# Optimization experiments

Hardware: AMD Instinct MI355X
Metric: run time of the kernel (lower is better)

Reference implementation:

```python
import jax, jax.numpy as jnp
import numpy as np

HEADS, DIM_HEAD, K_NN, EMB = 4, 64, 16, 256
INNER = HEADS * DIM_HEAD  # 256
POS_HID = 64
ATTN_HID = 4 * DIM_HEAD  # per-head hidden of grouped 1x1 conv MLP


def setup_inputs() -> dict:
    key = jax.random.key(0)
    ks = jax.random.split(key, 16)
    b, n = 2, 4096
    s = 0.05
    inp = {
        "x": jax.random.normal(ks[0], (b, n, EMB), jnp.float32),
        "mask": jnp.ones((b, n), dtype=bool),
        "pos": jax.random.normal(ks[1], (b, n, 3), jnp.float32),
        # to_qkv (no bias)
        "Wqkv": jax.random.normal(ks[2], (EMB, 3 * INNER), jnp.float32) * s,
        # pos_mlp: Linear(3,64) -> ReLU -> Linear(64, inner)
        "Wp1": jax.random.normal(ks[3], (3, POS_HID), jnp.float32) * s,
        "bp1": jax.random.normal(ks[4], (POS_HID,), jnp.float32) * s,
        "Wp2": jax.random.normal(ks[5], (POS_HID, INNER), jnp.float32) * s,
        "bp2": jax.random.normal(ks[6], (INNER,), jnp.float32) * s,
        # attn_mlp: grouped 1x1 convs == per-head linears [h, d_in, d_out]
        "Wa1": jax.random.normal(ks[7], (HEADS, DIM_HEAD, ATTN_HID), jnp.float32) * s,
        "ba1": jax.random.normal(ks[8], (HEADS, ATTN_HID), jnp.float32) * s,
        "Wa2": jax.random.normal(ks[9], (HEADS, ATTN_HID, DIM_HEAD), jnp.float32) * s,
        "ba2": jax.random.normal(ks[10], (HEADS, DIM_HEAD), jnp.float32) * s,
        # to_out
        "Wo": jax.random.normal(ks[11], (INNER, EMB), jnp.float32) * s,
        "bo": jax.random.normal(ks[12], (EMB,), jnp.float32) * s,
    }
    return inp


def reference(x, mask, pos, Wqkv, Wp1, bp1, Wp2, bp2, Wa1, ba1, Wa2, ba2, Wo, bo):
    b, n, _ = x.shape
    h, dh = HEADS, DIM_HEAD

    qkv = x @ Wqkv                              # [b, n, 3*inner]
    q, k, v = jnp.split(qkv, 3, axis=-1)
    to_heads = lambda t: t.reshape(b, n, h, dh).transpose(0, 2, 1, 3)  # [b,h,n,d]
    q, k, v = to_heads(q), to_heads(k), to_heads(v)

    # kNN on pos (per batch, squared euclidean, includes self)
    sq = jnp.sum(pos * pos, axis=-1)
    d2 = sq[:, :, None] + sq[:, None, :] - 2.0 * jnp.einsum('bid,bjd->bij', pos, pos)
    idx = jax.lax.top_k(-d2, K_NN)[1]            # [b, n, K]

    gat_h = jax.vmap(lambda t, i: t[:, i])       # [h,n,d],[n,K] -> [h,n,K,d]
    gat = jax.vmap(lambda t, i: t[i])            # [n,c],[n,K]  -> [n,K,c]

    qg = gat_h(q, idx)                           # [b,h,n,K,d]
    kg = gat_h(k, idx)
    vg = gat_h(v, idx)

    rel = gat(pos, idx) - pos[:, :, None, :]     # [b,n,K,3]
    rpe = jax.nn.relu(rel @ Wp1 + bp1) @ Wp2 + bp2               # [b,n,K,inner]
    rpe = rpe.reshape(b, n, K_NN, h, dh).transpose(0, 3, 1, 2, 4)  # [b,h,n,K,d]

    attn_in = qg - kg + rpe                      # [b,h,n,K,d]
    hid = jax.nn.relu(jnp.einsum('bhnkd,hde->bhnke', attn_in, Wa1)
                      + ba1[None, :, None, None, :])
    sim = (jnp.einsum('bhnke,hed->bhnkd', hid, Wa2)
           + ba2[None, :, None, None, :])        # [b,h,n,K,d]

    mg = jax.vmap(lambda m, i: m[i])(mask, idx)  # [b,n,K]
    pair = (mask[:, :, None] & mg)[:, None, :, :, None]
    sim = jnp.where(pair, sim, -jnp.finfo(sim.dtype).max)

    attn = jax.nn.softmax(sim, axis=3)           # over neighbors j
    # F.normalize over dim=-2 of [b,(h d),i,j] == over the point axis i
    attn = attn / jnp.maximum(jnp.linalg.norm(attn, axis=2, keepdims=True), 1e-12)

    agg = jnp.sum(attn * (vg + rpe), axis=3)     # [b,h,n,d]
    agg = agg.transpose(0, 2, 1, 3).reshape(b, n, h * dh)
    return agg @ Wo + bo
```

## Files before the change

kernel.cpp:

```cpp
#include <hip/hip_runtime.h>
#include <float.h>

typedef unsigned int uint;
typedef unsigned short ushort;

typedef _Float16 f16x8 __attribute__((ext_vector_type(8)));
typedef float f32x4 __attribute__((ext_vector_type(4)));
#define MFMA_F16(A, B, C) __builtin_amdgcn_mfma_f32_16x16x32_f16(A, B, C, 0, 0, 0)

__device__ __forceinline__ ushort f2h(float f) {
    _Float16 h = (_Float16)f;
    return __builtin_bit_cast(ushort, h);
}
__device__ __forceinline__ float h2f(ushort u) {
    _Float16 h = __builtin_bit_cast(_Float16, u);
    return (float)h;
}
__device__ __forceinline__ uint pack2(float a, float b) {
    return (uint)f2h(a) | ((uint)f2h(b) << 16);
}
__device__ __forceinline__ uint pkrtz(float a, float b) {
    return __builtin_bit_cast(uint, __builtin_amdgcn_cvt_pkrtz(a, b));
}
__device__ __forceinline__ f16x8 cast8(uint4 u) {
    return __builtin_bit_cast(f16x8, u);
}

template <int CTRL>
__device__ __forceinline__ void dpp_min(float& v, int& j) {
    int vp = __builtin_amdgcn_update_dpp(__float_as_int(v), __float_as_int(v),
                                         CTRL, 0xF, 0xF, false);
    int jp = __builtin_amdgcn_update_dpp(j, j, CTRL, 0xF, 0xF, false);
    float vf = __int_as_float(vp);
    bool better = (vf < v) || (vf == v && jp < j);
    v = better ? vf : v;
    j = better ? jp : j;
}
__device__ __forceinline__ void wave_min(float& v, int& j) {
    dpp_min<0x121>(v, j);
    dpp_min<0x122>(v, j);
    dpp_min<0x124>(v, j);
    dpp_min<0x128>(v, j);
    float ov = __shfl_xor(v, 16);
    int oj = __shfl_xor(j, 16);
    bool better = (ov < v) || (ov == v && oj < j);
    v = better ? ov : v;
    j = better ? oj : j;
    ov = __shfl_xor(v, 32);
    oj = __shfl_xor(j, 32);
    better = (ov < v) || (ov == v && oj < j);
    v = better ? ov : v;
    j = better ? oj : j;
}

__global__ void prep_kernel(const float* __restrict__ Wqkv, const float* __restrict__ Wa1,
                            const float* __restrict__ Wa2, const float* __restrict__ Wo,
                            const float* __restrict__ Wp2, const float* __restrict__ ba1,
                            ushort* __restrict__ WcatT, ushort* __restrict__ Wa1T,
                            ushort* __restrict__ Wa2T, ushort* __restrict__ WoT,
                            ushort* __restrict__ Wp2T, ushort* __restrict__ ba1p) {
    int t = blockIdx.x * 256 + threadIdx.x;
    {
        int cc2 = t >> 8, kk = t & 255;
        float val;
        if (cc2 < 256) val = Wqkv[kk * 768 + cc2] - Wqkv[kk * 768 + 256 + cc2];
        else           val = Wqkv[kk * 768 + 256 + cc2];
        WcatT[t] = f2h(val);
    }
    if (t < 65536) {
        int hh = t >> 14, r = t & 16383;
        int e = r >> 6, kin = r & 63;
        Wa1T[t] = f2h(Wa1[((size_t)(hh * 64 + kin)) * 256 + e]);
        int d = r >> 8, pos = r & 255;
        int ec = pos >> 5, lg = (pos >> 3) & 3, q = pos & 7;
        int e2 = ec * 32 + ((q >> 2) & 1) * 16 + lg * 4 + (q & 3);
        Wa2T[t] = f2h(Wa2[((size_t)(hh * 256 + e2)) * 64 + d]);
        int c3 = t >> 8, k3 = t & 255;
        WoT[t] = f2h(Wo[k3 * 256 + c3]);
    }
    if (t < 16384) {
        int row = t >> 6, p = t & 63;
        int h = row >> 6, s = row & 63;
        int ct = s >> 4, rr = s & 15;
        int d = (ct >> 1) * 32 + ((rr >> 2) & 3) * 8 + (ct & 1) * 4 + (rr & 3);
        Wp2T[t] = f2h(Wp2[p * 256 + h * 64 + d]);
    }
    if (t < 1024) {
        int h = t >> 8, pos = t & 255;
        int ec = pos >> 5, lg = (pos >> 3) & 3, q = pos & 7;
        int e2 = ec * 32 + ((q >> 2) & 1) * 16 + lg * 4 + (q & 3);
        ba1p[t] = f2h(ba1[h * 256 + e2]);
    }
}

__global__ void pos4_kernel(const float* __restrict__ pos, float4* __restrict__ pos4) {
    int t = blockIdx.x * 256 + threadIdx.x;
    float x = pos[t * 3 + 0], y = pos[t * 3 + 1], z = pos[t * 3 + 2];
    float4 o = {x, y, z, x * x + y * y + z * z};
    pos4[t] = o;
}

template <int MODE>
__global__ __launch_bounds__(256)
void hgemm(const void* __restrict__ Av, const ushort* __restrict__ Bt,
           const float* __restrict__ bias, void* __restrict__ C0v, ushort* __restrict__ C1h) {
    __shared__ ushort Af[64 * 40];
    __shared__ ushort Bf[128 * 40];
    const int tid = threadIdx.x;
    const int l = tid & 63, wv = tid >> 6;
    const int lg = l >> 4, lr = l & 15;
    const int row0 = blockIdx.x * 64, col0 = blockIdx.y * 128;
    const int mrow = (wv >> 1) * 32, ncol = (wv & 1) * 64;
    f32x4 acc[2][4];
#pragma unroll
    for (int mt = 0; mt < 2; ++mt)
#pragma unroll
        for (int nt = 0; nt < 4; ++nt) acc[mt][nt] = (f32x4){0.f, 0.f, 0.f, 0.f};

    for (int kk = 0; kk < 256; kk += 32) {
        if (MODE == 0) {
            const float* A = (const float*)Av;
            int r = tid >> 2, kq = (tid & 3) * 8;
            float4 a0 = *(const float4*)&A[(size_t)(row0 + r) * 256 + kk + kq];
            float4 a1 = *(const float4*)&A[(size_t)(row0 + r) * 256 + kk + kq + 4];
            uint4 u;
            u.x = pack2(a0.x, a0.y); u.y = pack2(a0.z, a0.w);
            u.z = pack2(a1.x, a1.y); u.w = pack2(a1.z, a1.w);
            *(uint4*)&Af[r * 40 + kq] = u;
        } else {
            const ushort* Ah = (const ushort*)Av;
            int r = tid >> 2, kq = (tid & 3) * 8;
            *(uint4*)&Af[r * 40 + kq] = *(const uint4*)&Ah[(size_t)(row0 + r) * 256 + kk + kq];
        }
        {
            int r = tid >> 1, hh = (tid & 1) * 16;
            const uint4* src = (const uint4*)&Bt[(size_t)(col0 + r) * 256 + kk + hh];
            uint4 b0 = src[0], b1 = src[1];
            *(uint4*)&Bf[r * 40 + hh] = b0;
            *(uint4*)&Bf[r * 40 + hh + 8] = b1;
        }
        __syncthreads();
        f16x8 afr[2], bfr[4];
#pragma unroll
        for (int mt = 0; mt < 2; ++mt)
            afr[mt] = *(const f16x8*)&Af[(mrow + mt * 16 + lr) * 40 + lg * 8];
#pragma unroll
        for (int nt = 0; nt < 4; ++nt)
            bfr[nt] = *(const f16x8*)&Bf[(ncol + nt * 16 + lr) * 40 + lg * 8];
#pragma unroll
        for (int mt = 0; mt < 2; ++mt)
#pragma unroll
            for (int nt = 0; nt < 4; ++nt)
                acc[mt][nt] = MFMA_F16(afr[mt], bfr[nt], acc[mt][nt]);
        __syncthreads();
    }
#pragma unroll
    for (int mt = 0; mt < 2; ++mt)
#pragma unroll
        for (int nt = 0; nt < 4; ++nt)
#pragma unroll
            for (int j = 0; j < 4; ++j) {
                int m = row0 + mrow + mt * 16 + lg * 4 + j;
                int n = col0 + ncol + nt * 16 + lr;
                float v = acc[mt][nt][j];
                if (MODE == 1) {
                    ((float*)C0v)[(size_t)m * 256 + n] = v + bias[n];
                } else {
                    int b = m >> 12, i2 = m & 4095;
                    if (n < 256) {
                        int hh = n >> 6, d = n & 63;
                        ((ushort*)C0v)[((size_t)((b * 4 + hh) << 12) + i2) * 64 + d] = f2h(v);
                    } else {
                        int n2 = n - 256;
                        int hh = n2 >> 6, d = n2 & 63;
                        C1h[((size_t)((b * 4 + hh) << 12) + i2) * 64 + d] = f2h(v);
                    }
                }
            }
}

__global__ __launch_bounds__(256, 6)
void knn_kernel(const float4* __restrict__ pos4, int* __restrict__ idx_out) {
    const int tid = threadIdx.x;
    const int lane = tid & 63, wv = tid >> 6;
    const int pblk = blockIdx.x;
    const int b = pblk >> 10;
    const int i = ((pblk & 1023) << 2) + wv;
    const float4* p4 = pos4 + (size_t)b * 4096;
    float4 pi = p4[i];
    float xi = pi.x, yi = pi.y, zi = pi.z, sqi = pi.w;
    const int SENT = 0x7fffffff;

    float v1[4], v2[4];
    int j1[4], j2[4];
#pragma unroll
    for (int g = 0; g < 4; ++g) { v1[g] = FLT_MAX; v2[g] = FLT_MAX; j1[g] = SENT; j2[g] = SENT; }
#pragma unroll 4
    for (int m = 0; m < 64; ++m) {
        int j = m * 64 + lane;
        float4 pj = p4[j];
        float v = sqi + pj.w - 2.f * (xi * pj.x + yi * pj.y + zi * pj.z);
        int g = m & 3;
        bool bb1 = (v < v1[g]) || (v == v1[g] && j < j1[g]);
        bool bb2 = (v < v2[g]) || (v == v2[g] && j < j2[g]);
        float nv2 = bb1 ? v1[g] : (bb2 ? v : v2[g]);
        int   nj2 = bb1 ? j1[g] : (bb2 ? j : j2[g]);
        v1[g] = bb1 ? v : v1[g];
        j1[g] = bb1 ? j : j1[g];
        v2[g] = nv2;
        j2[g] = nj2;
    }
    auto mergef = [](float& a1, int& aj1, float& a2, int& aj2,
                     float b1v, int bj1, float b2v, int bj2) {
        bool aFirst = (a1 < b1v) || (a1 == b1v && aj1 < bj1);
        float r1 = aFirst ? a1 : b1v;
        int rj1 = aFirst ? aj1 : bj1;
        float cand = aFirst ? a2 : b2v;
        int candj = aFirst ? aj2 : bj2;
        float oth = aFirst ? b1v : a1;
        int othj = aFirst ? bj1 : aj1;
        bool second = (cand < oth) || (cand == oth && candj < othj);
        a1 = r1; aj1 = rj1;
        a2 = second ? cand : oth;
        aj2 = second ? candj : othj;
    };
    mergef(v1[0], j1[0], v2[0], j2[0], v1[1], j1[1], v2[1], j2[1]);
    mergef(v1[2], j1[2], v2[2], j2[2], v1[3], j1[3], v2[3], j2[3]);
    mergef(v1[0], j1[0], v2[0], j2[0], v1[2], j1[2], v2[2], j2[2]);
    float c1v = v1[0], c2v = v2[0];
    int c1j = j1[0], c2j = j2[0];

    unsigned long long extr = 0ull;
    int keep = 0;
#pragma unroll 1
    for (int r = 0; r < 16; ++r) {
        float bv = c1v;
        int bj = c1j;
        wave_min(bv, bj);
        if (lane == r) keep = bj;
        int c = bj & 63;
        if (lane == (bj >> 6)) extr |= (1ull << c);
        if (lane == c) {
            c1v = c2v; c1j = c2j;
            c2v = FLT_MAX; c2j = SENT;
        }
        unsigned long long need = __ballot(lane == c && c1j == SENT);
        if (need) {
            int j = lane * 64 + c;
            float4 pj = p4[j];
            float v = sqi + pj.w - 2.f * (xi * pj.x + yi * pj.y + zi * pj.z);
            bool dead = (((extr >> c) & 1ull) != 0ull);
            v = dead ? FLT_MAX : v;
            float w1 = v; int wj1 = j;
            wave_min(w1, wj1);
            float w2 = (j == wj1) ? FLT_MAX : v;
            int wj2 = (j == wj1) ? SENT : j;
            wave_min(w2, wj2);
            if (lane == c) { c1v = w1; c1j = wj1; c2v = w2; c2j = wj2; }
        }
    }
    if (lane < 16)
        idx_out[((size_t)b * 4096 + i) * 16 + lane] = keep;
}

__global__ __launch_bounds__(256)
void attn_mfma(const ushort* __restrict__ qmkh, const ushort* __restrict__ vbufh,
               const float4* __restrict__ pos4, const int* __restrict__ idxb,
               const ushort* __restrict__ Wa1Tg, const ushort* __restrict__ Wa2Tg,
               const ushort* __restrict__ Wp2Tg, const ushort* __restrict__ ba1p,
               const float* __restrict__ ba2,
               const float* __restrict__ Wp1, const float* __restrict__ bp1,
               const float* __restrict__ bp2,
               ushort* __restrict__ prodbuf, float* __restrict__ part) {
    __shared__ ushort W1[256 * 72];
    __shared__ ushort W2[64 * 264];
    __shared__ ushort scr[4][16 * 88];
    const int tid = threadIdx.x;
    const int l = tid & 63, wv = tid >> 6;
    const int lg = l >> 4, lr = l & 15;
    const int c = blockIdx.x;
    const int h = c >> 8, rc = c & 255, b = rc >> 7, chunk = rc & 127;
    const int bh = b * 4 + h;

    {
        const uint4* g1 = (const uint4*)(Wa1Tg + (size_t)h * 16384);
        const uint4* g2 = (const uint4*)(Wa2Tg + (size_t)h * 16384);
#pragma unroll
        for (int it = 0; it < 8; ++it) {
            int ci = it * 256 + tid;
            *(uint4*)&W1[(ci >> 3) * 72 + (ci & 7) * 8] = g1[ci];
        }
#pragma unroll
        for (int it = 0; it < 8; ++it) {
            int ci = it * 256 + tid;
            *(uint4*)&W2[(ci >> 5) * 264 + (ci & 31) * 8] = g2[ci];
        }
    }
    __syncthreads();

    float b2v[4];
#pragma unroll
    for (int dt = 0; dt < 4; ++dt) b2v[dt] = ba2[h * 64 + dt * 16 + lr];

    f16x8 wp2f[4][2];
#pragma unroll
    for (int ct = 0; ct < 4; ++ct)
#pragma unroll
        for (int kt = 0; kt < 2; ++kt)
            wp2f[ct][kt] = *(const f16x8*)&Wp2Tg[(size_t)(h * 64 + ct * 16 + lr) * 64 + kt * 32 + lg * 8];
    f16x8 wp1h[3][2], bp1h[2], bp2h[2];
#pragma unroll
    for (int cc = 0; cc < 3; ++cc)
#pragma unroll
        for (int kt = 0; kt < 2; ++kt) {
            float4 w0 = *(const float4*)&Wp1[cc * 64 + kt * 32 + lg * 8];
            float4 w1 = *(const float4*)&Wp1[cc * 64 + kt * 32 + lg * 8 + 4];
            f16x8 wv8;
            wv8[0] = (_Float16)w0.x; wv8[1] = (_Float16)w0.y;
            wv8[2] = (_Float16)w0.z; wv8[3] = (_Float16)w0.w;
            wv8[4] = (_Float16)w1.x; wv8[5] = (_Float16)w1.y;
            wv8[6] = (_Float16)w1.z; wv8[7] = (_Float16)w1.w;
            wp1h[cc][kt] = wv8;
        }
#pragma unroll
    for (int kt = 0; kt < 2; ++kt) {
        float4 b0 = *(const float4*)&bp1[kt * 32 + lg * 8];
        float4 b1 = *(const float4*)&bp1[kt * 32 + lg * 8 + 4];
        f16x8 bv8;
        bv8[0] = (_Float16)b0.x; bv8[1] = (_Float16)b0.y;
        bv8[2] = (_Float16)b0.z; bv8[3] = (_Float16)b0.w;
        bv8[4] = (_Float16)b1.x; bv8[5] = (_Float16)b1.y;
        bv8[6] = (_Float16)b1.z; bv8[7] = (_Float16)b1.w;
        bp1h[kt] = bv8;
        float4 c0 = *(const float4*)&bp2[h * 64 + kt * 32 + lg * 8];
        float4 c1 = *(const float4*)&bp2[h * 64 + kt * 32 + lg * 8 + 4];
        f16x8 cv8;
        cv8[0] = (_Float16)c0.x; cv8[1] = (_Float16)c0.y;
        cv8[2] = (_Float16)c0.z; cv8[3] = (_Float16)c0.w;
        cv8[4] = (_Float16)c1.x; cv8[5] = (_Float16)c1.y;
        cv8[6] = (_Float16)c1.z; cv8[7] = (_Float16)c1.w;
        bp2h[kt] = cv8;
    }
    const float4* pb4 = pos4 + (size_t)b * 4096;
    const ushort* qbase = qmkh + (size_t)bh * 4096 * 64;
    const ushort* vbase = vbufh + (size_t)bh * 4096 * 64;
    const ushort* b1base = ba1p + h * 256;
    ushort* sw = &scr[wv][0];

    float asq[4][4];
#pragma unroll
    for (int dt = 0; dt < 4; ++dt)
#pragma unroll
        for (int j2 = 0; j2 < 4; ++j2) asq[dt][j2] = 0.f;

    for (int pg = 0; pg < 2; ++pg) {
        const int i0 = chunk * 32 + pg * 16 + wv * 4;
        int jj[4];
        f16x8 ain[4][2], rpef[4][2];
#pragma unroll
        for (int pp = 0; pp < 4; ++pp) {
            int i = i0 + pp;
            int row = ((b << 12) + i) * 16 + lr;
            int j = idxb[row];
            jj[pp] = j;
            float4 pj = pb4[j];
            float4 pi = pb4[i];
            _Float16 rxh = (_Float16)(pj.x - pi.x);
            _Float16 ryh = (_Float16)(pj.y - pi.y);
            _Float16 rzh = (_Float16)(pj.z - pi.z);
            f16x8 hf[2];
#pragma unroll
            for (int kt = 0; kt < 2; ++kt) {
                f16x8 t = bp1h[kt] + rxh * wp1h[0][kt] + ryh * wp1h[1][kt] + rzh * wp1h[2][kt];
#pragma unroll
                for (int q = 0; q < 8; ++q) t[q] = t[q] > (_Float16)0.f ? t[q] : (_Float16)0.f;
                hf[kt] = t;
            }
            f32x4 z4 = {0.f, 0.f, 0.f, 0.f};
            f32x4 racc[4];
#pragma unroll
            for (int ct = 0; ct < 4; ++ct) {
                racc[ct] = MFMA_F16(wp2f[ct][0], hf[0], z4);
                racc[ct] = MFMA_F16(wp2f[ct][1], hf[1], racc[ct]);
            }
            const ushort* qb = qbase + ((size_t)j) * 64 + lg * 8;
#pragma unroll
            for (int kt = 0; kt < 2; ++kt) {
                uint4 rp;
                rp.x = pkrtz(racc[2 * kt][0], racc[2 * kt][1]);
                rp.y = pkrtz(racc[2 * kt][2], racc[2 * kt][3]);
                rp.z = pkrtz(racc[2 * kt + 1][0], racc[2 * kt + 1][1]);
                rp.w = pkrtz(racc[2 * kt + 1][2], racc[2 * kt + 1][3]);
                f16x8 rv = cast8(rp) + bp2h[kt];
                rpef[pp][kt] = rv;
                f16x8 qv = *(const f16x8*)(qb + kt * 32);
                ain[pp][kt] = qv + rv;
            }
        }
        f32x4 acc[4][4];
#pragma unroll
        for (int pp = 0; pp < 4; ++pp)
#pragma unroll
            for (int dt = 0; dt < 4; ++dt) acc[pp][dt] = (f32x4){0.f, 0.f, 0.f, 0.f};

        for (int ec = 0; ec < 8; ++ec) {
            f16x8 A1[2][2], B2f[4];
#pragma unroll
            for (int et = 0; et < 2; ++et)
#pragma unroll
                for (int kt = 0; kt < 2; ++kt)
                    A1[et][kt] = *(const f16x8*)&W1[(ec * 32 + et * 16 + lr) * 72 + kt * 32 + lg * 8];
#pragma unroll
            for (int dt = 0; dt < 4; ++dt)
                B2f[dt] = *(const f16x8*)&W2[(dt * 16 + lr) * 264 + ec * 32 + lg * 8];
            f16x8 b1h = *(const f16x8*)&b1base[ec * 32 + lg * 8];
#pragma unroll
            for (int pp = 0; pp < 4; ++pp) {
                f32x4 z = {0.f, 0.f, 0.f, 0.f};
                f32x4 h0 = MFMA_F16(A1[0][0], ain[pp][0], z);
                h0 = MFMA_F16(A1[0][1], ain[pp][1], h0);
                f32x4 h1 = MFMA_F16(A1[1][0], ain[pp][0], z);
                h1 = MFMA_F16(A1[1][1], ain[pp][1], h1);
                uint4 hp;
                hp.x = pkrtz(h0[0], h0[1]); hp.y = pkrtz(h0[2], h0[3]);
                hp.z = pkrtz(h1[0], h1[1]); hp.w = pkrtz(h1[2], h1[3]);
                f16x8 hv = cast8(hp) + b1h;
#pragma unroll
                for (int q = 0; q < 8; ++q) hv[q] = hv[q] > (_Float16)0.f ? hv[q] : (_Float16)0.f;
#pragma unroll
                for (int dt = 0; dt < 4; ++dt)
                    acc[pp][dt] = MFMA_F16(hv, B2f[dt], acc[pp][dt]);
            }
        }
#pragma unroll
        for (int pp = 0; pp < 4; ++pp) {
            int i = i0 + pp;
            float at[4][4];
#pragma unroll
            for (int dt = 0; dt < 4; ++dt) {
                float e0 = __expf(acc[pp][dt][0] + b2v[dt]);
                float e1 = __expf(acc[pp][dt][1] + b2v[dt]);
                float e2 = __expf(acc[pp][dt][2] + b2v[dt]);
                float e3 = __expf(acc[pp][dt][3] + b2v[dt]);
                float s = e0 + e1 + e2 + e3;
                s += __shfl_xor(s, 16);
                s += __shfl_xor(s, 32);
                float is = 1.f / s;
                at[dt][0] = e0 * is; at[dt][1] = e1 * is;
                at[dt][2] = e2 * is; at[dt][3] = e3 * is;
                asq[dt][0] += at[dt][0] * at[dt][0];
                asq[dt][1] += at[dt][1] * at[dt][1];
                asq[dt][2] += at[dt][2] * at[dt][2];
                asq[dt][3] += at[dt][3] * at[dt][3];
            }
#pragma unroll
            for (int dt = 0; dt < 4; ++dt) {
                sw[(lg * 4 + 0) * 88 + dt * 16 + lr] = f2h(at[dt][0]);
                sw[(lg * 4 + 1) * 88 + dt * 16 + lr] = f2h(at[dt][1]);
                sw[(lg * 4 + 2) * 88 + dt * 16 + lr] = f2h(at[dt][2]);
                sw[(lg * 4 + 3) * 88 + dt * 16 + lr] = f2h(at[dt][3]);
            }
            const ushort* vb = vbase + (size_t)jj[pp] * 64 + lg * 8;
            ushort* pr = prodbuf + ((size_t)(bh * 4096 + i) * 16 + lr) * 64 + lg * 8;
#pragma unroll
            for (int kt = 0; kt < 2; ++kt) {
                f16x8 atB = *(const f16x8*)&sw[lr * 88 + kt * 32 + lg * 8];
                f16x8 vv = *(const f16x8*)(vb + kt * 32);
                f16x8 p = (vv + rpef[pp][kt]) * atB;
                *(f16x8*)(pr + kt * 32) = p;
            }
        }
    }
    float* scrF = (float*)&scr[0][0];
#pragma unroll
    for (int dt = 0; dt < 4; ++dt) {
        __syncthreads();
#pragma unroll
        for (int j2 = 0; j2 < 4; ++j2)
            scrF[wv * 288 + lr * 18 + lg * 4 + j2] = asq[dt][j2];
        __syncthreads();
        int fr = tid >> 4, fk = tid & 15;
        float s = scrF[fr * 18 + fk] + scrF[288 + fr * 18 + fk] +
                  scrF[576 + fr * 18 + fk] + scrF[864 + fr * 18 + fk];
        part[((size_t)c * 4 + dt) * 256 + tid] = s;
    }
}

__global__ void inv_kernel(const float* __restrict__ part, float* __restrict__ invn) {
    int t = blockIdx.x * 256 + threadIdx.x;
    int bh = t >> 10, f = t & 1023;
    int d = f >> 4, k = f & 15;
    int dt = d >> 4, lr = d & 15;
    int cbase = (bh & 3) * 256 + (bh >> 2) * 128;
    float s = 0.f;
    for (int cc = 0; cc < 128; ++cc)
        s += part[((size_t)(cbase + cc) * 4 + dt) * 256 + lr * 16 + k];
    invn[t] = 1.f / fmaxf(sqrtf(s), 1e-12f);
}

__global__ void finalize_kernel(const ushort* __restrict__ prodbuf, const float* __restrict__ invn,
                                ushort* __restrict__ aggh) {
    int t = blockIdx.x * 256 + threadIdx.x;
    int d = t & 63;
    int i = (t >> 6) & 4095;
    int bh = t >> 18;
    const ushort* pr = prodbuf + ((size_t)(bh * 4096 + i)) * 1024 + d;
    const float* iv = invn + bh * 1024 + d * 16;
    float accv = 0.f;
#pragma unroll
    for (int k = 0; k < 16; ++k)
        accv += h2f(pr[(size_t)k * 64]) * iv[k];
    int hh = bh & 3, bb = bh >> 2;
    aggh[((size_t)(bb * 4096 + i)) * 256 + hh * 64 + d] = f2h(accv);
}

extern "C" void kernel_launch(void* const* d_in, const int* in_sizes, int n_in,
                              void* d_out, int out_size, void* d_ws, size_t ws_size,
                              hipStream_t stream) {
    const float* x    = (const float*)d_in[0];
    const float* pos  = (const float*)d_in[2];
    const float* Wqkv = (const float*)d_in[3];
    const float* Wp1  = (const float*)d_in[4];
    const float* bp1  = (const float*)d_in[5];
    const float* Wp2  = (const float*)d_in[6];
    const float* bp2  = (const float*)d_in[7];
    const float* Wa1  = (const float*)d_in[8];
    const float* ba1  = (const float*)d_in[9];
    const float* Wa2  = (const float*)d_in[10];
    const float* ba2  = (const float*)d_in[11];
    const float* Wo   = (const float*)d_in[12];
    const float* bo   = (const float*)d_in[13];

    char* base = (char*)d_ws;
    size_t off = 0;
    auto carve = [&](size_t bytes) -> char* {
        char* r = base + off;
        off = (off + bytes + 255) & ~(size_t)255;
        return r;
    };
    ushort* qmkh   = (ushort*)carve(4194304);
    ushort* vbufh  = (ushort*)carve(4194304);
    ushort* WcatT  = (ushort*)carve(262144);
    ushort* Wa1Tg  = (ushort*)carve(131072);
    ushort* Wa2Tg  = (ushort*)carve(131072);
    ushort* WoT    = (ushort*)carve(131072);
    ushort* Wp2Tg  = (ushort*)carve(32768);
    ushort* ba1pg  = (ushort*)carve(2048);
    float4* pos4   = (float4*)carve(131072);
    int*    idx    = (int*)carve(524288);
    ushort* prodbuf= (ushort*)carve(67108864);
    float*  part   = (float*)carve(4194304);
    float*  invn   = (float*)carve(32768);
    ushort* aggh   = (ushort*)carve(4194304);

    prep_kernel<<<512, 256, 0, stream>>>(Wqkv, Wa1, Wa2, Wo, Wp2, ba1,
                                         WcatT, Wa1Tg, Wa2Tg, WoT, Wp2Tg, ba1pg);
    pos4_kernel<<<32, 256, 0, stream>>>(pos, pos4);
    hgemm<0><<<dim3(128, 4), 256, 0, stream>>>(x, WcatT, nullptr, qmkh, vbufh);
    knn_kernel<<<2048, 256, 0, stream>>>(pos4, idx);
    attn_mfma<<<1024, 256, 0, stream>>>(qmkh, vbufh, pos4, idx, Wa1Tg, Wa2Tg, Wp2Tg, ba1pg,
                                        ba2, Wp1, bp1, bp2, prodbuf, part);
    inv_kernel<<<32, 256, 0, stream>>>(part, invn);
    finalize_kernel<<<8192, 256, 0, stream>>>(prodbuf, invn, aggh);
    hgemm<1><<<dim3(128, 2), 256, 0, stream>>>(aggh, WoT, bo, d_out, nullptr);
}
```

Measured before the change: 183.0 us.

## Cache kNN distances in LDS and scan contiguous column segments per lane

The kNN kernel now writes all 4096 squared distances for each query into a padded per-wave LDS tile. Each lane then scans its own contiguous 64-candidate segment, tracking two top-2 lists instead of four. Refills during the 16-round extraction read distances back from LDS instead of reloading positions and recomputing them, and extracted entries are marked by writing FLT_MAX rather than kept in a bitmask. Blocks shrink to 2 waves to fit 33KB of LDS, and block-wide syncs are added inside the extraction loop, which may reduce occupancy and add barrier cost.

```diff
diff --git a/kernel.cpp b/kernel.cpp
--- a/kernel.cpp
+++ b/kernel.cpp
@@ -179,28 +179,38 @@
             }
 }
 
-__global__ __launch_bounds__(256, 6)
+__global__ __launch_bounds__(128)
 void knn_kernel(const float4* __restrict__ pos4, int* __restrict__ idx_out) {
+    __shared__ float ds2[2][65 * 64];
     const int tid = threadIdx.x;
     const int lane = tid & 63, wv = tid >> 6;
     const int pblk = blockIdx.x;
-    const int b = pblk >> 10;
-    const int i = ((pblk & 1023) << 2) + wv;
+    const int b = pblk >> 11;
+    const int i = ((pblk & 2047) << 1) + wv;
     const float4* p4 = pos4 + (size_t)b * 4096;
     float4 pi = p4[i];
     float xi = pi.x, yi = pi.y, zi = pi.z, sqi = pi.w;
+    float* ds = ds2[wv];
     const int SENT = 0x7fffffff;
 
-    float v1[4], v2[4];
-    int j1[4], j2[4];
-#pragma unroll
-    for (int g = 0; g < 4; ++g) { v1[g] = FLT_MAX; v2[g] = FLT_MAX; j1[g] = SENT; j2[g] = SENT; }
-#pragma unroll 4
+#pragma unroll 8
     for (int m = 0; m < 64; ++m) {
         int j = m * 64 + lane;
         float4 pj = p4[j];
         float v = sqi + pj.w - 2.f * (xi * pj.x + yi * pj.y + zi * pj.z);
-        int g = m & 3;
+        ds[m * 65 + lane] = v;
+    }
+    __syncthreads();
+
+    float v1[2], v2[2];
+    int j1[2], j2[2];
+#pragma unroll
+    for (int g = 0; g < 2; ++g) { v1[g] = FLT_MAX; v2[g] = FLT_MAX; j1[g] = SENT; j2[g] = SENT; }
+#pragma unroll 8
+    for (int m = 0; m < 64; ++m) {
+        float v = ds[lane * 65 + m];
+        int j = lane * 64 + m;
+        int g = m & 1;
         bool bb1 = (v < v1[g]) || (v == v1[g] && j < j1[g]);
         bool bb2 = (v < v2[g]) || (v == v2[g] && j < j2[g]);
         float nv2 = bb1 ? v1[g] : (bb2 ? v : v2[g]);
@@ -210,27 +220,21 @@
         v2[g] = nv2;
         j2[g] = nj2;
     }
-    auto mergef = [](float& a1, int& aj1, float& a2, int& aj2,
-                     float b1v, int bj1, float b2v, int bj2) {
-        bool aFirst = (a1 < b1v) || (a1 == b1v && aj1 < bj1);
-        float r1 = aFirst ? a1 : b1v;
-        int rj1 = aFirst ? aj1 : bj1;
-        float cand = aFirst ? a2 : b2v;
-        int candj = aFirst ? aj2 : bj2;
-        float oth = aFirst ? b1v : a1;
-        int othj = aFirst ? bj1 : aj1;
+    float c1v, c2v;
+    int c1j, c2j;
+    {
+        bool aFirst = (v1[0] < v1[1]) || (v1[0] == v1[1] && j1[0] < j1[1]);
+        c1v = aFirst ? v1[0] : v1[1];
+        c1j = aFirst ? j1[0] : j1[1];
+        float cand = aFirst ? v2[0] : v2[1];
+        int candj = aFirst ? j2[0] : j2[1];
+        float oth = aFirst ? v1[1] : v1[0];
+        int othj = aFirst ? j1[1] : j1[0];
         bool second = (cand < oth) || (cand == oth && candj < othj);
-        a1 = r1; aj1 = rj1;
-        a2 = second ? cand : oth;
-        aj2 = second ? candj : othj;
-    };
-    mergef(v1[0], j1[0], v2[0], j2[0], v1[1], j1[1], v2[1], j2[1]);
-    mergef(v1[2], j1[2], v2[2], j2[2], v1[3], j1[3], v2[3], j2[3]);
-    mergef(v1[0], j1[0], v2[0], j2[0], v1[2], j1[2], v2[2], j2[2]);
-    float c1v = v1[0], c2v = v2[0];
-    int c1j = j1[0], c2j = j2[0];
-
-    unsigned long long extr = 0ull;
+        c2v = second ? cand : oth;
+        c2j = second ? candj : othj;
+    }
+
     int keep = 0;
 #pragma unroll 1
     for (int r = 0; r < 16; ++r) {
@@ -238,19 +242,17 @@
         int bj = c1j;
         wave_min(bv, bj);
         if (lane == r) keep = bj;
-        int c = bj & 63;
-        if (lane == (bj >> 6)) extr |= (1ull << c);
+        int c = bj >> 6;
+        if (lane == 0) ds[c * 65 + (bj & 63)] = FLT_MAX;
         if (lane == c) {
             c1v = c2v; c1j = c2j;
             c2v = FLT_MAX; c2j = SENT;
         }
+        __syncthreads();
         unsigned long long need = __ballot(lane == c && c1j == SENT);
         if (need) {
-            int j = lane * 64 + c;
-            float4 pj = p4[j];
-            float v = sqi + pj.w - 2.f * (xi * pj.x + yi * pj.y + zi * pj.z);
-            bool dead = (((extr >> c) & 1ull) != 0ull);
-            v = dead ? FLT_MAX : v;
+            float v = ds[c * 65 + lane];
+            int j = c * 64 + lane;
             float w1 = v; int wj1 = j;
             wave_min(w1, wj1);
             float w2 = (j == wj1) ? FLT_MAX : v;
@@ -557,7 +559,7 @@
                                          WcatT, Wa1Tg, Wa2Tg, WoT, Wp2Tg, ba1pg);
     pos4_kernel<<<32, 256, 0, stream>>>(pos, pos4);
     hgemm<0><<<dim3(128, 4), 256, 0, stream>>>(x, WcatT, nullptr, qmkh, vbufh);
-    knn_kernel<<<2048, 256, 0, stream>>>(pos4, idx);
+    knn_kernel<<<4096, 128, 0, stream>>>(pos4, idx);
     attn_mfma<<<1024, 256, 0, stream>>>(qmkh, vbufh, pos4, idx, Wa1Tg, Wa2Tg, Wp2Tg, ba1pg,
                                         ba2, Wp1, bp1, bp2, prodbuf, part);
     inv_kernel<<<32, 256, 0, stream>>>(part, invn);
```

Result: slower. 237.4 us (+29.7%).
